# Kernel optimization log

Measured on AMD Instinct MI355X. Metric: run time of the kernel, lower is better.

Reference implementation:

```python
import jax, jax.numpy as jnp
import numpy as np
import math

B, T, D, H = 4, 1024, 1024, 16
DK = D // H
EPS = 1e-12  # F.normalize eps

def setup_inputs() -> dict:
    key = jax.random.key(0)
    ks = jax.random.split(key, 6)
    xav = math.sqrt(6.0 / (D + D))  # xavier_uniform bound for square Linear
    x = jax.random.normal(ks[0], (B, T, D), dtype=jnp.float32)
    Wq = jax.random.uniform(ks[1], (D, D), jnp.float32, -xav, xav)
    Wk = jax.random.uniform(ks[2], (D, D), jnp.float32, -xav, xav)
    Wv = jax.random.uniform(ks[3], (D, D), jnp.float32, -xav, xav)
    Wo = jax.random.uniform(ks[4], (D, D), jnp.float32, -xav, xav)
    logit_g = math.log(0.9 / 0.1)
    logit_l = math.log(0.1 / 0.9)
    W_gamma = jnp.zeros((H,), jnp.float32)
    b_gamma = jnp.full((H,), logit_g, jnp.float32)
    W_lambda = jnp.zeros((H,), jnp.float32)
    b_lambda = jnp.full((H,), logit_l, jnp.float32)
    return {"x": x, "Wq": Wq, "Wk": Wk, "Wv": Wv, "Wo": Wo,
            "W_gamma": W_gamma, "b_gamma": b_gamma,
            "W_lambda": W_lambda, "b_lambda": b_lambda}

def reference(x, Wq, Wk, Wv, Wo, W_gamma, b_gamma, W_lambda, b_lambda):
    b, t, d = x.shape
    # projections (torch Linear: x @ W.T), split heads -> [T, B, H, dk] for scan
    def proj(W):
        return jnp.einsum('btd,ed->bte', x, W).reshape(b, t, H, DK).transpose(1, 0, 2, 3)
    q = proj(Wq)
    k = proj(Wk)
    v = proj(Wv)
    # L2-normalize k along dk (F.normalize semantics)
    k = k / jnp.maximum(jnp.linalg.norm(k, axis=-1, keepdims=True), EPS)
    k_bar = k.mean(axis=-1)  # [T, B, H]
    gamma = jax.nn.sigmoid(W_gamma * k_bar + b_gamma)
    lam = jax.nn.sigmoid(W_lambda * k_bar + b_lambda)
    rho = (1.0 - lam) * gamma  # [T, B, H]

    S0 = jnp.zeros((b, H, DK, DK), x.dtype)

    def step(S, inp):
        q_t, k_t, v_t, rho_t = inp  # [B,H,dk] x3, [B,H]
        r = rho_t[..., None, None]
        S = r * S + (1.0 - r) * jnp.einsum('bhv,bhk->bhvk', v_t, k_t)
        y_t = jnp.einsum('bhv,bhvk->bhk', q_t, S)
        return S, y_t

    _, ys = jax.lax.scan(step, S0, (q, k, v, rho))  # ys: [T, B, H, dk]
    out = ys.transpose(1, 0, 2, 3).reshape(b, t, d)
    return jnp.einsum('btd,ed->bte', out, Wo)
```

## Files before the change

kernel.cpp:

```cpp
#include <hip/hip_runtime.h>
#include <hip/hip_bf16.h>


typedef __bf16 b16x8 __attribute__((ext_vector_type(8)));
typedef float  f32x4 __attribute__((ext_vector_type(4)));
typedef unsigned short u16x8 __attribute__((ext_vector_type(8)));
using bf16_t = __hip_bfloat16;

#define AS1C(p) ((const __attribute__((address_space(1))) void*)(p))
#define AS3(p)  ((__attribute__((address_space(3))) void*)(p))

__device__ __forceinline__ void g2l16(const void* g, void* l) {
  __builtin_amdgcn_global_load_lds(AS1C(g), AS3(l), 16, 0, 0);
}
__device__ __forceinline__ void g2l4(const void* g, void* l) {
  __builtin_amdgcn_global_load_lds(AS1C(g), AS3(l), 4, 0, 0);
}

__device__ __forceinline__ unsigned short f2b(float x) {
  unsigned u = __float_as_uint(x);
  return (unsigned short)((u + 0x7FFFu + ((u >> 16) & 1u)) >> 16);
}
__device__ __forceinline__ float b2f(unsigned short b) {
  return __uint_as_float(((unsigned)b) << 16);
}

__device__ __forceinline__ int wire_flag(const unsigned* __restrict__ x, int tid) {
  unsigned u = x[tid & 63];
  int e = (int)((u >> 23) & 0xFF);
  unsigned long long m = __ballot(e >= 95 && e <= 135);
  return (__popcll(m) >= 32) ? 1 : 0;
}

__global__ __launch_bounds__(256)
void convert_all(const void* __restrict__ x,
                 const void* __restrict__ w0, const void* __restrict__ w1,
                 const void* __restrict__ w2, const void* __restrict__ w3,
                 unsigned short* __restrict__ xb,
                 unsigned short* __restrict__ wb0, unsigned short* __restrict__ wb1,
                 unsigned short* __restrict__ wb2, unsigned short* __restrict__ wb3)
{
  const int fm = wire_flag((const unsigned*)x, threadIdx.x);
  const long i8 = ((long)blockIdx.x * 256 + threadIdx.x) * 8;
  const void* src; unsigned short* dst; long off;
  if (i8 < 4194304) { src = x; dst = xb; off = i8; }
  else {
    long j = i8 - 4194304;
    int w = (int)(j >> 20); off = j & 1048575;
    src = (w == 0) ? w0 : (w == 1) ? w1 : (w == 2) ? w2 : w3;
    dst = (w == 0) ? wb0 : (w == 1) ? wb1 : (w == 2) ? wb2 : wb3;
  }
  if (fm) {
    const float4 a = *(const float4*)((const float*)src + off);
    const float4 b = *(const float4*)((const float*)src + off + 4);
    u16x8 o;
    o[0] = f2b(a.x); o[1] = f2b(a.y); o[2] = f2b(a.z); o[3] = f2b(a.w);
    o[4] = f2b(b.x); o[5] = f2b(b.y); o[6] = f2b(b.z); o[7] = f2b(b.w);
    *(u16x8*)(dst + off) = o;
  } else {
    *(int4*)(dst + off) = *(const int4*)((const unsigned short*)src + off);
  }
}

__global__ __launch_bounds__(256)
void gemm_qkv(const unsigned* __restrict__ xraw,
              const bf16_t* __restrict__ A,
              const bf16_t* __restrict__ B0, const bf16_t* __restrict__ B1,
              const bf16_t* __restrict__ B2,
              unsigned short* __restrict__ C0, unsigned short* __restrict__ C1,
              unsigned short* __restrict__ C2,
              const void* __restrict__ Wg, const void* __restrict__ bg,
              const void* __restrict__ Wl, const void* __restrict__ bl,
              float* __restrict__ rho)
{
  constexpr int K = 1024, N = 1024;
  const int flat = blockIdx.x;
  const int xcd = flat & 7, sl = flat >> 3;
  const int z = sl >> 5, t5 = sl & 31;
  const int bx = ((xcd & 1) << 2) | (t5 & 3);
  const int by = ((xcd >> 1) << 3) | (t5 >> 2);
  const bf16_t* B = (z == 0) ? B0 : (z == 1) ? B1 : B2;
  unsigned short* C = (z == 0) ? C0 : (z == 1) ? C1 : C2;
  __shared__ __align__(16) unsigned short As[128 * 64];
  __shared__ __align__(16) unsigned short Bs[128 * 64];
  const int tid  = threadIdx.x;
  const int lane = tid & 63;
  const int wave = tid >> 6;
  const int wm = wave >> 1, wn = wave & 1;
  const int quad = lane >> 4, tm = lane & 15;
  const long row0 = (long)by * 128;
  const long col0 = (long)bx * 128;

  f32x4 acc[4][4];
#pragma unroll
  for (int i = 0; i < 4; ++i)
#pragma unroll
    for (int j = 0; j < 4; ++j) acc[i][j] = (f32x4){0.f, 0.f, 0.f, 0.f};

  const int sr = tid >> 3;
  const int c2 = tid & 7;
  const int gc = c2 ^ (sr & 7);
  const bf16_t* ap = A + (row0 + sr) * (long)K + gc * 8;
  const bf16_t* bp = B + (col0 + sr) * (long)K + gc * 8;
  unsigned short* la = As + tid * 8;
  unsigned short* lb = Bs + tid * 8;

  for (int kt = 0; kt < K; kt += 64) {
    __syncthreads();
#pragma unroll
    for (int sh = 0; sh < 4; ++sh) {
      g2l16(ap + (long)sh * 32 * K + kt, la + sh * 2048);
      g2l16(bp + (long)sh * 32 * K + kt, lb + sh * 2048);
    }
    __syncthreads();

#pragma unroll
    for (int kk = 0; kk < 2; ++kk) {
      const int pcsel = ((kk * 4 + quad) ^ (tm & 7)) << 3;
      b16x8 af[4], bfr[4];
#pragma unroll
      for (int i = 0; i < 4; ++i)
        af[i] = *(const b16x8*)&As[(wm * 64 + i * 16 + tm) * 64 + pcsel];
#pragma unroll
      for (int j = 0; j < 4; ++j)
        bfr[j] = *(const b16x8*)&Bs[(wn * 64 + j * 16 + tm) * 64 + pcsel];
#pragma unroll
      for (int i = 0; i < 4; ++i)
#pragma unroll
        for (int j = 0; j < 4; ++j)
          acc[i][j] = __builtin_amdgcn_mfma_f32_16x16x32_bf16(af[i], bfr[j], acc[i][j], 0, 0, 0);
    }
  }

  if (z != 1) {
#pragma unroll
    for (int i = 0; i < 4; ++i)
#pragma unroll
      for (int j = 0; j < 4; ++j)
#pragma unroll
        for (int r = 0; r < 4; ++r) {
          long row = row0 + wm * 64 + i * 16 + quad * 4 + r;
          long col = col0 + wn * 64 + j * 16 + tm;
          C[row * N + col] = f2b(acc[i][j][r]);
        }
  } else {
    const int fm = wire_flag(xraw, tid);
    const int h = bx * 2 + wn;
    float wgv, bgv, wlv, blv;
    if (fm) {
      wgv = ((const float*)Wg)[h]; bgv = ((const float*)bg)[h];
      wlv = ((const float*)Wl)[h]; blv = ((const float*)bl)[h];
    } else {
      wgv = b2f(((const unsigned short*)Wg)[h]); bgv = b2f(((const unsigned short*)bg)[h]);
      wlv = b2f(((const unsigned short*)Wl)[h]); blv = b2f(((const unsigned short*)bl)[h]);
    }
#pragma unroll
    for (int i = 0; i < 4; ++i)
#pragma unroll
      for (int r = 0; r < 4; ++r) {
        float ss = 0.f, sv = 0.f;
#pragma unroll
        for (int j = 0; j < 4; ++j) {
          const float v = acc[i][j][r];
          ss += v * v; sv += v;
        }
#pragma unroll
        for (int m = 1; m < 16; m <<= 1) {
          ss += __shfl_xor(ss, m);
          sv += __shfl_xor(sv, m);
        }
        const float inv = 1.f / fmaxf(sqrtf(ss), 1e-12f);
        const long row = row0 + wm * 64 + i * 16 + quad * 4 + r;
#pragma unroll
        for (int j = 0; j < 4; ++j)
          C[row * N + col0 + wn * 64 + j * 16 + tm] = f2b(acc[i][j][r] * inv);
        if (tm == 0) {
          const float kbar = sv * inv * (1.f / 64.f);
          const float gm = 1.f / (1.f + expf(-(wgv * kbar + bgv)));
          const float lm = 1.f / (1.f + expf(-(wlv * kbar + blv)));
          const int b = (int)(row >> 10), t = (int)(row & 1023);
          rho[(size_t)(b * 16 + h) * 1024 + t] = (1.f - lm) * gm;
        }
      }
  }
}

__global__ __launch_bounds__(256)
void gemm_out64(const unsigned* __restrict__ xraw,
                const bf16_t* __restrict__ A, const bf16_t* __restrict__ B,
                void* __restrict__ C)
{
  constexpr int K = 1024, N = 1024;
  const int flat = blockIdx.x;
  const int xcd = flat & 7, sl = flat >> 3;
  const int bx = sl & 15;
  const int by = (xcd << 3) | (sl >> 4);
  __shared__ __align__(16) unsigned short As[64 * 64];
  __shared__ __align__(16) unsigned short Bs[64 * 64];
  const int tid  = threadIdx.x;
  const int lane = tid & 63;
  const int wave = tid >> 6;
  const int quad = lane >> 4, tm = lane & 15;
  const long row0 = (long)by * 64;
  const long col0 = (long)bx * 64;

  f32x4 acc[4];
#pragma unroll
  for (int i = 0; i < 4; ++i) acc[i] = (f32x4){0.f, 0.f, 0.f, 0.f};

  const int sr = tid >> 2;
  const int scc = tid & 3;
  const int qg = (scc - (sr >> 1)) & 3;
  const bf16_t* ap = A + (row0 + sr) * (long)K + qg * 8;
  const bf16_t* bp = B + (col0 + sr) * (long)K + qg * 8;
  unsigned short* la = As + tid * 8;
  unsigned short* lb = Bs + tid * 8;
  const int cc = (quad + ((tm >> 1) & 3)) & 3;

  for (int kt = 0; kt < K; kt += 64) {
    __syncthreads();
    g2l16(ap + kt,      la);
    g2l16(ap + kt + 32, la + 2048);
    g2l16(bp + kt,      lb);
    g2l16(bp + kt + 32, lb + 2048);
    __syncthreads();

    b16x8 bf0 = *(const b16x8*)&Bs[(wave * 16 + tm) * 32 + cc * 8];
    b16x8 bf1 = *(const b16x8*)&Bs[2048 + (wave * 16 + tm) * 32 + cc * 8];
#pragma unroll
    for (int i = 0; i < 4; ++i) {
      b16x8 a0 = *(const b16x8*)&As[(i * 16 + tm) * 32 + cc * 8];
      b16x8 a1 = *(const b16x8*)&As[2048 + (i * 16 + tm) * 32 + cc * 8];
      acc[i] = __builtin_amdgcn_mfma_f32_16x16x32_bf16(a0, bf0, acc[i], 0, 0, 0);
      acc[i] = __builtin_amdgcn_mfma_f32_16x16x32_bf16(a1, bf1, acc[i], 0, 0, 0);
    }
  }

  const int fm = wire_flag(xraw, tid);
#pragma unroll
  for (int i = 0; i < 4; ++i)
#pragma unroll
    for (int r = 0; r < 4; ++r) {
      const long row = row0 + i * 16 + quad * 4 + r;
      const long col = col0 + wave * 16 + tm;
      const float v = acc[i][r];
      if (fm) ((float*)C)[row * N + col] = v;
      else    ((unsigned short*)C)[row * N + col] = f2b(v);
    }
}

__device__ __forceinline__ void stage_chunk_x(const unsigned short* G, int n0c, int h,
                                              unsigned short* lds, int tid) {
#pragma unroll
  for (int sh = 0; sh < 2; ++sh) {
    const int idx = sh * 256 + tid;
    const int row = idx >> 3, c2 = idx & 7;
    const int gc = c2 ^ (row & 7);
    g2l16(G + (size_t)(n0c + row) * 1024 + h * 64 + gc * 8, lds + idx * 8);
  }
}
__device__ __forceinline__ void stage_blk_x(const unsigned short* G,
                                            unsigned short* lds, int tid) {
#pragma unroll
  for (int sh = 0; sh < 2; ++sh) {
    const int idx = sh * 256 + tid;
    const int row = idx >> 3, c2 = idx & 7;
    const int gc = c2 ^ (row & 7);
    g2l16(G + row * 64 + gc * 8, lds + idx * 8);
  }
}
__device__ __forceinline__ b16x8 rdx(const unsigned short* lds, int row, int k0) {
  return *(const b16x8*)&lds[row * 64 + (((k0 >> 3) ^ (row & 7)) << 3)];
}
__device__ __forceinline__ float rdx1(const unsigned short* lds, int row, int col) {
  return b2f(lds[row * 64 + (((col >> 3) ^ (row & 7)) << 3) + (col & 7)]);
}

__device__ __forceinline__ void transpose_x(const unsigned short* src,
                                            unsigned short* dst,
                                            const float* sc, int tid) {
  const int kc = tid & 63;
  const int s4 = (tid >> 6) * 16;
  u16x8 o0, o1;
#pragma unroll
  for (int i = 0; i < 16; ++i) {
    const int s = s4 + i;
    float v = rdx1(src, s, kc);
    if (sc) v *= sc[s];
    const unsigned short b = f2b(v);
    if (i < 8) o0[i] = b; else o1[i - 8] = b;
  }
  *(u16x8*)&dst[kc * 72 + s4]     = o0;
  *(u16x8*)&dst[kc * 72 + s4 + 8] = o1;
}

__device__ __forceinline__ void rho_scan(const float* rho_s, float* aw, float* cw,
                                         float* sc, int tid) {
  if (tid < 64) {
    const float r = rho_s[tid];
    float p = r;
#pragma unroll
    for (int d = 1; d < 64; d <<= 1) {
      float o = __shfl_up(p, d);
      if (tid >= d) p *= o;
    }
    aw[tid] = p;
    const float c = (1.f - r) / p;
    cw[tid] = c;
    const float Ac = __shfl(p, 63);
    sc[tid] = Ac * c;
  }
}

__global__ __launch_bounds__(256)
void chunk_outer(const unsigned short* __restrict__ Kb, const unsigned short* __restrict__ Vb,
                 const float* __restrict__ rho, unsigned short* __restrict__ Ug,
                 float* __restrict__ A_g)
{
  __shared__ __align__(16) unsigned short ks[4096];
  __shared__ __align__(16) unsigned short vs[4096];
  __shared__ __align__(16) unsigned short kt[64 * 72];
  __shared__ __align__(16) unsigned short vt[64 * 72];
  __shared__ float rho_s[64], aw[64], cw[64], sc[64];
  const int tid = threadIdx.x;
  const int bid = blockIdx.x;
  const int bh = bid >> 4, c = bid & 15;
  const int b = bh >> 4, h = bh & 15;
  const int n0c = b * 1024 + c * 64;
  const int lane = tid & 63, wave = tid >> 6;
  const int quad = lane >> 4, tm = lane & 15;

  stage_chunk_x(Kb, n0c, h, ks, tid);
  stage_chunk_x(Vb, n0c, h, vs, tid);
  if (tid < 64) g2l4(rho + (size_t)bh * 1024 + c * 64 + tid, rho_s + tid);
  __syncthreads();
  rho_scan(rho_s, aw, cw, sc, tid);
  __syncthreads();
  transpose_x(ks, kt, sc, tid);
  transpose_x(vs, vt, nullptr, tid);
  __syncthreads();

  const int mrow = 16 * wave + tm;
  b16x8 a0 = *(const b16x8*)&kt[mrow * 72 + quad * 8];
  b16x8 a1 = *(const b16x8*)&kt[mrow * 72 + 32 + quad * 8];
#pragma unroll
  for (int j4 = 0; j4 < 4; ++j4) {
    const int nrow = 16 * j4 + tm;
    b16x8 b0 = *(const b16x8*)&vt[nrow * 72 + quad * 8];
    b16x8 b1 = *(const b16x8*)&vt[nrow * 72 + 32 + quad * 8];
    f32x4 acc = (f32x4){0.f, 0.f, 0.f, 0.f};
    acc = __builtin_amdgcn_mfma_f32_16x16x32_bf16(a0, b0, acc, 0, 0, 0);
    acc = __builtin_amdgcn_mfma_f32_16x16x32_bf16(a1, b1, acc, 0, 0, 0);
#pragma unroll
    for (int r = 0; r < 4; ++r) {
      const int kc = 16 * wave + quad * 4 + r;
      Ug[(size_t)bid * 4096 + kc * 64 + 16 * j4 + tm] = f2b(acc[r]);
    }
  }
  if (tid == 0) A_g[bid] = aw[63];
}

__global__ __launch_bounds__(256)
void chunk_scan(const unsigned short* __restrict__ Ug, const float* __restrict__ A_g,
                unsigned short* __restrict__ Sp)
{
  const int bh = blockIdx.x >> 4;
  const int e  = (blockIdx.x & 15) * 256 + threadIdx.x;
  const size_t base = (size_t)bh * 16 * 4096 + e;
  float S = 0.f;
#pragma unroll
  for (int c = 0; c < 16; ++c) {
    Sp[base + (size_t)c * 4096] = f2b(S);
    S = A_g[bh * 16 + c] * S + b2f(Ug[base + (size_t)c * 4096]);
  }
}

__global__ __launch_bounds__(256)
void chunk_y(const unsigned short* __restrict__ Qb, const unsigned short* __restrict__ Kb,
             const unsigned short* __restrict__ Vb, const unsigned short* __restrict__ Sp,
             const float* __restrict__ rho, unsigned short* __restrict__ Yb)
{
  __shared__ __align__(16) unsigned short qs[4096];
  __shared__ __align__(16) unsigned short ks[4096];
  __shared__ __align__(16) unsigned short vs[4096];
  __shared__ __align__(16) unsigned short ss[4096];
  __shared__ __align__(16) unsigned short kt[64 * 72];
  __shared__ __align__(16) unsigned short pt[64 * 72];
  __shared__ float rho_s[64], aw[64], cw[64], sc[64];
  const int tid = threadIdx.x;
  const int bid = blockIdx.x;
  const int bh = bid >> 4, c = bid & 15;
  const int b = bh >> 4, h = bh & 15;
  const int n0c = b * 1024 + c * 64;
  const int lane = tid & 63, wave = tid >> 6;
  const int quad = lane >> 4, tm = lane & 15;

  stage_chunk_x(Qb, n0c, h, qs, tid);
  stage_chunk_x(Kb, n0c, h, ks, tid);
  stage_chunk_x(Vb, n0c, h, vs, tid);
  stage_blk_x(Sp + (size_t)bid * 4096, ss, tid);
  if (tid < 64) g2l4(rho + (size_t)bh * 1024 + c * 64 + tid, rho_s + tid);
  __syncthreads();
  rho_scan(rho_s, aw, cw, sc, tid);
  __syncthreads();
  transpose_x(ks, kt, nullptr, tid);

  __bf16* ptb = (__bf16*)pt;
  const int trow = 16 * wave + tm;

  b16x8 af_q[2];
#pragma unroll
  for (int kk = 0; kk < 2; ++kk)
    af_q[kk] = rdx(qs, trow, kk * 32 + quad * 8);
#pragma unroll
  for (int j4 = 0; j4 < 4; ++j4) {
    f32x4 acc = (f32x4){0.f, 0.f, 0.f, 0.f};
#pragma unroll
    for (int kk = 0; kk < 2; ++kk) {
      const b16x8 bf = rdx(vs, 16 * j4 + tm, kk * 32 + quad * 8);
      acc = __builtin_amdgcn_mfma_f32_16x16x32_bf16(af_q[kk], bf, acc, 0, 0, 0);
    }
    const int s = 16 * j4 + tm;
    const float cws = cw[s];
#pragma unroll
    for (int r = 0; r < 4; ++r) {
      const int t = 16 * wave + quad * 4 + r;
      const float w = (s <= t) ? aw[t] * cws : 0.f;
      ptb[t * 72 + s] = (__bf16)(acc[r] * w);
    }
  }

  const float at = aw[trow];
  b16x8 af_qs[2], af_p[2];
#pragma unroll
  for (int kk = 0; kk < 2; ++kk) {
    b16x8 t8;
#pragma unroll
    for (int j = 0; j < 8; ++j) t8[j] = (__bf16)(at * (float)af_q[kk][j]);
    af_qs[kk] = t8;
    af_p[kk] = *(const b16x8*)&pt[trow * 72 + kk * 32 + quad * 8];
  }
  __syncthreads();

#pragma unroll
  for (int j4 = 0; j4 < 4; ++j4) {
    const int kc = 16 * j4 + tm;
    f32x4 acc = (f32x4){0.f, 0.f, 0.f, 0.f};
#pragma unroll
    for (int kk = 0; kk < 2; ++kk) {
      const int kbase = kk * 32 + quad * 8;
      const b16x8 bk = *(const b16x8*)&kt[kc * 72 + kbase];
      const b16x8 bs = rdx(ss, kc, kbase);
      acc = __builtin_amdgcn_mfma_f32_16x16x32_bf16(af_p[kk],  bk, acc, 0, 0, 0);
      acc = __builtin_amdgcn_mfma_f32_16x16x32_bf16(af_qs[kk], bs, acc, 0, 0, 0);
    }
#pragma unroll
    for (int r = 0; r < 4; ++r) {
      const int t = 16 * wave + quad * 4 + r;
      Yb[(size_t)(n0c + t) * 1024 + h * 64 + kc] = f2b(acc[r]);
    }
  }
}

extern "C" void kernel_launch(void* const* d_in, const int* in_sizes, int n_in,
                              void* d_out, int out_size, void* d_ws, size_t ws_size,
                              hipStream_t stream) {
  const void* x  = d_in[0];
  const void* Wq = d_in[1];
  const void* Wk = d_in[2];
  const void* Wv = d_in[3];
  const void* Wo = d_in[4];

  char* ws = (char*)d_ws;
  const size_t MB = 1ull << 20;
  unsigned short* x_b  = (unsigned short*)(ws);
  unsigned short* Wq_b = (unsigned short*)(ws + 8 * MB);
  unsigned short* Wk_b = (unsigned short*)(ws + 10 * MB);
  unsigned short* Wv_b = (unsigned short*)(ws + 12 * MB);
  unsigned short* Wo_b = (unsigned short*)(ws + 14 * MB);
  unsigned short* Qb = (unsigned short*)(ws + 16 * MB);
  unsigned short* Kb = (unsigned short*)(ws + 24 * MB);
  unsigned short* Vb = (unsigned short*)(ws + 32 * MB);
  unsigned short* Yb = (unsigned short*)(ws + 40 * MB);
  unsigned short* Ug = (unsigned short*)(ws + 48 * MB);
  unsigned short* Sp = (unsigned short*)(ws + 64 * MB);
  float*  rh   = (float*)(ws + 72 * MB);
  float*  A_g  = (float*)(ws + 72 * MB + 256 * 1024);

  dim3 blk(256);
  convert_all<<<dim3(4096), blk, 0, stream>>>(x, Wq, Wk, Wv, Wo,
                                              x_b, Wq_b, Wk_b, Wv_b, Wo_b);
  gemm_qkv<<<dim3(768), blk, 0, stream>>>((const unsigned*)x,
      (const bf16_t*)x_b, (const bf16_t*)Wq_b, (const bf16_t*)Wk_b, (const bf16_t*)Wv_b,
      Qb, Kb, Vb, d_in[5], d_in[6], d_in[7], d_in[8], rh);
  chunk_outer<<<dim3(1024), blk, 0, stream>>>(Kb, Vb, rh, Ug, A_g);
  chunk_scan<<<dim3(1024), blk, 0, stream>>>(Ug, A_g, Sp);
  chunk_y<<<dim3(1024), blk, 0, stream>>>(Qb, Kb, Vb, Sp, rh, Yb);
  gemm_out64<<<dim3(1024), blk, 0, stream>>>((const unsigned*)x,
      (const bf16_t*)Yb, (const bf16_t*)Wo_b, d_out);
}
```

Baseline: 164.3 us.

## Double GEMM K-tile with XOR swizzle and trim syncs in chunk kernels

The output GEMM now stages 128-wide K tiles instead of 64, using an XOR swizzle that matches the MFMA read pattern. This halves the number of barrier-separated load/compute iterations at the cost of twice the LDS per block. In chunk_outer and chunk_y, rho is read straight from global memory into the prefix-product scan instead of being staged asynchronously into LDS first. chunk_outer applies the K scaling to MFMA operands in registers after the transpose, and the chunk kernels each drop one barrier.

Measured after the change: 165.6 us. About the same (+0.8%).

```diff
diff --git a/kernel.cpp b/kernel.cpp
--- a/kernel.cpp
+++ b/kernel.cpp
@@ -12,9 +12,6 @@
 
 __device__ __forceinline__ void g2l16(const void* g, void* l) {
   __builtin_amdgcn_global_load_lds(AS1C(g), AS3(l), 16, 0, 0);
-}
-__device__ __forceinline__ void g2l4(const void* g, void* l) {
-  __builtin_amdgcn_global_load_lds(AS1C(g), AS3(l), 4, 0, 0);
 }
 
 __device__ __forceinline__ unsigned short f2b(float x) {
@@ -195,8 +192,8 @@
   const int xcd = flat & 7, sl = flat >> 3;
   const int bx = sl & 15;
   const int by = (xcd << 3) | (sl >> 4);
-  __shared__ __align__(16) unsigned short As[64 * 64];
-  __shared__ __align__(16) unsigned short Bs[64 * 64];
+  __shared__ __align__(16) unsigned short As[64 * 128];
+  __shared__ __align__(16) unsigned short Bs[64 * 128];
   const int tid  = threadIdx.x;
   const int lane = tid & 63;
   const int wave = tid >> 6;
@@ -208,31 +205,31 @@
 #pragma unroll
   for (int i = 0; i < 4; ++i) acc[i] = (f32x4){0.f, 0.f, 0.f, 0.f};
 
-  const int sr = tid >> 2;
-  const int scc = tid & 3;
-  const int qg = (scc - (sr >> 1)) & 3;
-  const bf16_t* ap = A + (row0 + sr) * (long)K + qg * 8;
-  const bf16_t* bp = B + (col0 + sr) * (long)K + qg * 8;
+  const int sr16 = tid >> 4;
+  const int gc = (tid & 15) ^ sr16;
+  const bf16_t* ap = A + (row0 + sr16) * (long)K + gc * 8;
+  const bf16_t* bp = B + (col0 + sr16) * (long)K + gc * 8;
   unsigned short* la = As + tid * 8;
   unsigned short* lb = Bs + tid * 8;
-  const int cc = (quad + ((tm >> 1) & 3)) & 3;
-
-  for (int kt = 0; kt < K; kt += 64) {
+
+  for (int kt = 0; kt < K; kt += 128) {
     __syncthreads();
-    g2l16(ap + kt,      la);
-    g2l16(ap + kt + 32, la + 2048);
-    g2l16(bp + kt,      lb);
-    g2l16(bp + kt + 32, lb + 2048);
+#pragma unroll
+    for (int sh = 0; sh < 4; ++sh) {
+      g2l16(ap + (long)sh * 16 * K + kt, la + sh * 2048);
+      g2l16(bp + (long)sh * 16 * K + kt, lb + sh * 2048);
+    }
     __syncthreads();
 
-    b16x8 bf0 = *(const b16x8*)&Bs[(wave * 16 + tm) * 32 + cc * 8];
-    b16x8 bf1 = *(const b16x8*)&Bs[2048 + (wave * 16 + tm) * 32 + cc * 8];
-#pragma unroll
-    for (int i = 0; i < 4; ++i) {
-      b16x8 a0 = *(const b16x8*)&As[(i * 16 + tm) * 32 + cc * 8];
-      b16x8 a1 = *(const b16x8*)&As[2048 + (i * 16 + tm) * 32 + cc * 8];
-      acc[i] = __builtin_amdgcn_mfma_f32_16x16x32_bf16(a0, bf0, acc[i], 0, 0, 0);
-      acc[i] = __builtin_amdgcn_mfma_f32_16x16x32_bf16(a1, bf1, acc[i], 0, 0, 0);
+#pragma unroll
+    for (int kk = 0; kk < 4; ++kk) {
+      const int slot = (((kk << 2) | quad) ^ tm) << 3;
+      b16x8 bfv = *(const b16x8*)&Bs[(wave * 16 + tm) * 128 + slot];
+#pragma unroll
+      for (int i = 0; i < 4; ++i) {
+        b16x8 afv = *(const b16x8*)&As[(i * 16 + tm) * 128 + slot];
+        acc[i] = __builtin_amdgcn_mfma_f32_16x16x32_bf16(afv, bfv, acc[i], 0, 0, 0);
+      }
     }
   }
 
@@ -277,27 +274,23 @@
 }
 
 __device__ __forceinline__ void transpose_x(const unsigned short* src,
-                                            unsigned short* dst,
-                                            const float* sc, int tid) {
+                                            unsigned short* dst, int tid) {
   const int kc = tid & 63;
   const int s4 = (tid >> 6) * 16;
   u16x8 o0, o1;
 #pragma unroll
   for (int i = 0; i < 16; ++i) {
-    const int s = s4 + i;
-    float v = rdx1(src, s, kc);
-    if (sc) v *= sc[s];
-    const unsigned short b = f2b(v);
+    const unsigned short b = f2b(rdx1(src, s4 + i, kc));
     if (i < 8) o0[i] = b; else o1[i - 8] = b;
   }
   *(u16x8*)&dst[kc * 72 + s4]     = o0;
   *(u16x8*)&dst[kc * 72 + s4 + 8] = o1;
 }
 
-__device__ __forceinline__ void rho_scan(const float* rho_s, float* aw, float* cw,
-                                         float* sc, int tid) {
+__device__ __forceinline__ void rho_scan_g(const float* __restrict__ rho_g,
+                                           float* aw, float* cw, float* sc, int tid) {
   if (tid < 64) {
-    const float r = rho_s[tid];
+    const float r = rho_g[tid];
     float p = r;
 #pragma unroll
     for (int d = 1; d < 64; d <<= 1) {
@@ -307,8 +300,7 @@
     aw[tid] = p;
     const float c = (1.f - r) / p;
     cw[tid] = c;
-    const float Ac = __shfl(p, 63);
-    sc[tid] = Ac * c;
+    sc[tid] = __shfl(p, 63) * c;
   }
 }
 
@@ -321,7 +313,7 @@
   __shared__ __align__(16) unsigned short vs[4096];
   __shared__ __align__(16) unsigned short kt[64 * 72];
   __shared__ __align__(16) unsigned short vt[64 * 72];
-  __shared__ float rho_s[64], aw[64], cw[64], sc[64];
+  __shared__ float aw[64], cw[64], sc[64];
   const int tid = threadIdx.x;
   const int bid = blockIdx.x;
   const int bh = bid >> 4, c = bid & 15;
@@ -332,22 +324,27 @@
 
   stage_chunk_x(Kb, n0c, h, ks, tid);
   stage_chunk_x(Vb, n0c, h, vs, tid);
-  if (tid < 64) g2l4(rho + (size_t)bh * 1024 + c * 64 + tid, rho_s + tid);
   __syncthreads();
-  rho_scan(rho_s, aw, cw, sc, tid);
+  rho_scan_g(rho + (size_t)bh * 1024 + c * 64, aw, cw, sc, tid);
+  transpose_x(ks, kt, tid);
+  transpose_x(vs, vt, tid);
   __syncthreads();
-  transpose_x(ks, kt, sc, tid);
-  transpose_x(vs, vt, nullptr, tid);
-  __syncthreads();
 
   const int mrow = 16 * wave + tm;
-  b16x8 a0 = *(const b16x8*)&kt[mrow * 72 + quad * 8];
-  b16x8 a1 = *(const b16x8*)&kt[mrow * 72 + 32 + quad * 8];
+  const int kb0 = quad * 8;
+  const b16x8 kraw0 = *(const b16x8*)&kt[mrow * 72 + kb0];
+  const b16x8 kraw1 = *(const b16x8*)&kt[mrow * 72 + 32 + kb0];
+  b16x8 a0, a1;
+#pragma unroll
+  for (int j = 0; j < 8; ++j) {
+    a0[j] = (__bf16)(sc[kb0 + j] * (float)kraw0[j]);
+    a1[j] = (__bf16)(sc[32 + kb0 + j] * (float)kraw1[j]);
+  }
 #pragma unroll
   for (int j4 = 0; j4 < 4; ++j4) {
     const int nrow = 16 * j4 + tm;
-    b16x8 b0 = *(const b16x8*)&vt[nrow * 72 + quad * 8];
-    b16x8 b1 = *(const b16x8*)&vt[nrow * 72 + 32 + quad * 8];
+    b16x8 b0 = *(const b16x8*)&vt[nrow * 72 + kb0];
+    b16x8 b1 = *(const b16x8*)&vt[nrow * 72 + 32 + kb0];
     f32x4 acc = (f32x4){0.f, 0.f, 0.f, 0.f};
     acc = __builtin_amdgcn_mfma_f32_16x16x32_bf16(a0, b0, acc, 0, 0, 0);
     acc = __builtin_amdgcn_mfma_f32_16x16x32_bf16(a1, b1, acc, 0, 0, 0);
@@ -386,7 +383,7 @@
   __shared__ __align__(16) unsigned short ss[4096];
   __shared__ __align__(16) unsigned short kt[64 * 72];
   __shared__ __align__(16) unsigned short pt[64 * 72];
-  __shared__ float rho_s[64], aw[64], cw[64], sc[64];
+  __shared__ float aw[64], cw[64], sc[64];
   const int tid = threadIdx.x;
   const int bid = blockIdx.x;
   const int bh = bid >> 4, c = bid & 15;
@@ -399,11 +396,10 @@
   stage_chunk_x(Kb, n0c, h, ks, tid);
   stage_chunk_x(Vb, n0c, h, vs, tid);
   stage_blk_x(Sp + (size_t)bid * 4096, ss, tid);
-  if (tid < 64) g2l4(rho + (size_t)bh * 1024 + c * 64 + tid, rho_s + tid);
   __syncthreads();
-  rho_scan(rho_s, aw, cw, sc, tid);
+  rho_scan_g(rho + (size_t)bh * 1024 + c * 64, aw, cw, sc, tid);
+  transpose_x(ks, kt, tid);
   __syncthreads();
-  transpose_x(ks, kt, nullptr, tid);
 
   __bf16* ptb = (__bf16*)pt;
   const int trow = 16 * wave + tm;
@@ -440,7 +436,6 @@
     af_qs[kk] = t8;
     af_p[kk] = *(const b16x8*)&pt[trow * 72 + kk * 32 + quad * 8];
   }
-  __syncthreads();
 
 #pragma unroll
   for (int j4 = 0; j4 < 4; ++j4) {
```
